# Kernel optimization log

Measured on AMD Instinct MI355X. Metric: run time of the kernel, lower is better.

The kernel has to match this reference:

```python
import jax, jax.numpy as jnp
import numpy as np

BLOCK = 64      # BigBird block size
HEADS = 8
N_GLOBAL = 1
WINDOW = 1      # +/-1 block sliding window
N_RAND = 3


def _build_block_idx(n_blocks, seed=0):
    """Per query block: global + window + random key blocks, causal, deduped, -1 padded."""
    rng = np.random.RandomState(seed)
    m = N_GLOBAL + (2 * WINDOW + 1) + N_RAND  # 7
    idx = np.full((n_blocks, m), -1, np.int32)
    for i in range(n_blocks):
        s = set(range(min(N_GLOBAL, i + 1)))
        for w in range(i - WINDOW, i + 1):  # causal window (blocks <= i)
            if w >= 0:
                s.add(w)
        cand = [c for c in range(i + 1) if c not in s]
        rng.shuffle(cand)
        s.update(cand[:N_RAND])
        ss = sorted(s)
        idx[i, :len(ss)] = ss
    return idx


def setup_inputs() -> dict:
    key = jax.random.key(0)
    ks = jax.random.split(key, 12)
    b, S, D = 4, 4096, 768
    dff = 4 * D
    init = lambda k, shape: (0.02 * jax.random.normal(k, shape, jnp.float32))
    return {
        'q': jax.random.normal(ks[0], (b, S, D), jnp.float32),
        'ln1_g': jnp.ones((D,), jnp.float32), 'ln1_b': jnp.zeros((D,), jnp.float32),
        'Wq': init(ks[1], (D, D)), 'bq': jnp.zeros((D,), jnp.float32),
        'Wk': init(ks[2], (D, D)), 'bk': jnp.zeros((D,), jnp.float32),
        'Wv': init(ks[3], (D, D)), 'bv': jnp.zeros((D,), jnp.float32),
        'Wo': init(ks[4], (D, D)), 'bo': jnp.zeros((D,), jnp.float32),
        'ln2_g': jnp.ones((D,), jnp.float32), 'ln2_b': jnp.zeros((D,), jnp.float32),
        'W1': init(ks[5], (D, dff)), 'b1': jnp.zeros((dff,), jnp.float32),
        'W2': init(ks[6], (dff, D)), 'b2': jnp.zeros((D,), jnp.float32),
        'key_block_idx': jnp.asarray(_build_block_idx(S // BLOCK), jnp.int32),
    }


def _layernorm(x, g, b, eps=1e-5):
    mu = jnp.mean(x, axis=-1, keepdims=True)
    var = jnp.mean(jnp.square(x - mu), axis=-1, keepdims=True)
    return (x - mu) * jax.lax.rsqrt(var + eps) * g + b


def _bigbird_attn(x, Wq, bq, Wk, bk, Wv, bv, Wo, bo, key_block_idx):
    b, S, D = x.shape
    H, hd = HEADS, D // HEADS
    nb = S // BLOCK
    m = key_block_idx.shape[1]
    proj = lambda W, bias: (x @ W + bias).reshape(b, nb, BLOCK, H, hd).transpose(0, 3, 1, 2, 4)
    q = proj(Wq, bq)  # [b,h,nb,B,hd]
    k = proj(Wk, bk)
    v = proj(Wv, bv)
    valid = key_block_idx >= 0                      # [nb, m]
    idx = jnp.maximum(key_block_idx, 0)
    kg = k[:, :, idx]                               # [b,h,nb,m,B,hd]
    vg = v[:, :, idx]
    scores = jnp.einsum('bhnqd,bhnmkd->bhnqmk', q, kg) / jnp.sqrt(jnp.float32(hd))
    off = jnp.arange(BLOCK)
    qpos = jnp.arange(nb)[:, None] * BLOCK + off    # [nb, B]
    kpos = idx[..., None] * BLOCK + off             # [nb, m, B]
    mask = valid[:, :, None] & (kpos[:, None, :, :] <= qpos[:, :, None, None])  # [nb,q,m,k]
    scores = jnp.where(mask[None, None], scores, jnp.float32(-1e9))
    attn = jax.nn.softmax(scores.reshape(b, H, nb, BLOCK, m * BLOCK), axis=-1)
    attn = attn.reshape(b, H, nb, BLOCK, m, BLOCK)
    out = jnp.einsum('bhnqmk,bhnmkd->bhnqd', attn, vg)   # [b,h,nb,B,hd]
    out = out.transpose(0, 2, 3, 1, 4).reshape(b, S, D)
    return out @ Wo + bo


def reference(q, ln1_g, ln1_b, Wq, bq, Wk, bk, Wv, bv, Wo, bo,
              ln2_g, ln2_b, W1, b1, W2, b2, key_block_idx):
    # pre-norm residual: x + attn(ln1(x))
    x = q + _bigbird_attn(_layernorm(q, ln1_g, ln1_b), Wq, bq, Wk, bk, Wv, bv, Wo, bo, key_block_idx)
    h = _layernorm(x, ln2_g, ln2_b)
    x = x + (jax.nn.gelu(h @ W1 + b1) @ W2 + b2)
    return x
```

## Files before the change

kernel.cpp:

```cpp
#include <hip/hip_runtime.h>
#include <cstdint>

typedef __bf16  bf16x8 __attribute__((ext_vector_type(8)));
typedef float   f32x4  __attribute__((ext_vector_type(4)));

__device__ __forceinline__ float bf2f(uint16_t u) {
    uint32_t x = ((uint32_t)u) << 16;
    float f; __builtin_memcpy(&f, &x, 4); return f;
}
__device__ __forceinline__ uint16_t f2bf(float f) {
    uint32_t x; __builtin_memcpy(&x, &f, 4);
    uint32_t r = (x + 0x7fffu + ((x >> 16) & 1u)) >> 16;
    return (uint16_t)r;
}
__device__ __forceinline__ float gelu_f(float x) {
    float y = 0.7978845608028654f * (x + 0.044715f * x * x * x);
    float e = __expf(-2.0f * y);
    return x * __builtin_amdgcn_rcpf(1.0f + e);
}
__device__ __forceinline__ float ldf(const void* p, size_t i, int f) {
    return f ? ((const float*)p)[i] : bf2f(((const uint16_t*)p)[i]);
}

__device__ __forceinline__ void gl_lds16(const void* g, void* lds) {
    __builtin_amdgcn_global_load_lds(
        (const __attribute__((address_space(1))) void*)g,
        (__attribute__((address_space(3))) void*)lds,
        16, 0, 0);
}

#define BATCH 4
#define SEQ   4096
#define DMODEL 768
#define HEADS 8
#define HDIM  96
#define DFF   3072
#define NBLK  64
#define MKEYS 7
#define MROWS 16384

__global__ void sniff_k(const uint32_t* __restrict__ g, int* __restrict__ flag) {
    if (threadIdx.x == 0) flag[0] = (g[0] == 0x3F800000u) ? 1 : 0;
}

__global__ void transpose_k(const void* __restrict__ in, uint16_t* __restrict__ out,
                            int R, int C, const int* __restrict__ flag) {
    __shared__ float t[32][33];
    const int f = flag[0];
    int bx = blockIdx.x * 32, by = blockIdx.y * 32;
    int tx = threadIdx.x, ty = threadIdx.y;
    #pragma unroll
    for (int i = 0; i < 32; i += 8)
        t[ty + i][tx] = ldf(in, (size_t)(by + ty + i) * C + bx + tx, f);
    __syncthreads();
    #pragma unroll
    for (int i = 0; i < 32; i += 8)
        out[(size_t)(bx + ty + i) * R + by + tx] = f2bf(t[tx][ty + i]);
}

__global__ void concat_bias_k(const void* bq, const void* bk, const void* bv,
                              uint16_t* out, const int* __restrict__ flag) {
    const int f = flag[0];
    int i = blockIdx.x * 256 + threadIdx.x;
    if (i < DMODEL) {
        out[i]              = f2bf(ldf(bq, i, f));
        out[DMODEL + i]     = f2bf(ldf(bk, i, f));
        out[2 * DMODEL + i] = f2bf(ldf(bv, i, f));
    }
}

__global__ __launch_bounds__(256) void ln_k(const void* __restrict__ x,
                                            const void* __restrict__ g,
                                            const void* __restrict__ b,
                                            uint16_t* __restrict__ y,
                                            int xmode, const int* __restrict__ flag) {
    const int f = flag[0];
    const int xf = xmode ? f : 0;
    int row = blockIdx.x, tid = threadIdx.x;
    size_t base = (size_t)row * DMODEL;
    float v0 = ldf(x, base + tid, xf);
    float v1 = ldf(x, base + tid + 256, xf);
    float v2 = ldf(x, base + tid + 512, xf);
    float s = v0 + v1 + v2;
    float s2 = v0 * v0 + v1 * v1 + v2 * v2;
    #pragma unroll
    for (int off = 1; off < 64; off <<= 1) {
        s  += __shfl_xor(s, off, 64);
        s2 += __shfl_xor(s2, off, 64);
    }
    __shared__ float rs[4], rs2[4];
    if ((tid & 63) == 0) { rs[tid >> 6] = s; rs2[tid >> 6] = s2; }
    __syncthreads();
    s = rs[0] + rs[1] + rs[2] + rs[3];
    s2 = rs2[0] + rs2[1] + rs2[2] + rs2[3];
    float mu = s * (1.0f / DMODEL);
    float var = s2 * (1.0f / DMODEL) - mu * mu;
    float rstd = rsqrtf(var + 1e-5f);
    uint16_t* yr = y + base;
    yr[tid]       = f2bf((v0 - mu) * rstd * ldf(g, tid, f)       + ldf(b, tid, f));
    yr[tid + 256] = f2bf((v1 - mu) * rstd * ldf(g, tid + 256, f) + ldf(b, tid + 256, f));
    yr[tid + 512] = f2bf((v2 - mu) * rstd * ldf(g, tid + 512, f) + ldf(b, tid + 512, f));
}

template <int EPI>
__global__ __launch_bounds__(512, 4) void gemm128(
        const uint16_t* __restrict__ A, const uint16_t* __restrict__ Bt,
        const void* __restrict__ bias, const void* __restrict__ resid,
        void* __restrict__ C, int M, int N, int K,
        int bmode, int rmode, int omode, const int* __restrict__ flag) {
    __shared__ __align__(16) uint16_t SMEM[36864];
    const int f = flag[0];
    const int bf_ = bmode ? f : 0, rf = rmode ? f : 0, of = omode ? f : 0;
    const int tid = threadIdx.x;
    const int lane = tid & 63, wave = tid >> 6;
    const int l15 = lane & 15, quad = lane >> 4;
    const int wr = wave >> 2, wc = wave & 3;

    const int GX = gridDim.x;
    const int flat = blockIdx.y * GX + blockIdx.x;
    const int xcd = flat & 7, w8 = flat >> 3;
    const int cb = w8 % GX;
    const int rb = (w8 / GX) * 8 + xcd;
    const int m0 = rb * 128, n0 = cb * 256;
    const int NT = K >> 5;

    const uint32_t cxor = ((uint32_t)(quad ^ ((l15 >> 2) & 3))) << 4;
    const uint32_t aA = (uint32_t)((wr * 64 + l15) * 64) + cxor;
    const uint32_t aB = 24576u + (uint32_t)((wc * 64 + l15) * 64) + cxor;
    const char* const smb = (const char*)SMEM;

    const uint32_t goffA = (uint32_t)((tid >> 2) * K + (((tid & 3) ^ ((tid >> 4) & 3)) << 3));

    f32x4 acc[4][4] = {};
    bf16x8 af[4], bfr[4];

    const uint16_t* const Abase = A + (size_t)m0 * K;
    const uint16_t* const Bbase = Bt + (size_t)n0 * K;

    auto stage = [&](int t, int s) {
        const uint16_t* ga = Abase + t * 32 + goffA;
        const uint16_t* gb = Bbase + t * 32 + goffA;
        uint16_t* da = SMEM + s * 4096 + wave * 512;
        uint16_t* db = SMEM + 12288 + s * 8192 + wave * 512;
        gl_lds16(ga, da);
        gl_lds16(gb, db);
        gl_lds16(gb + (size_t)128 * K, db + 4096);
    };

#define LD(S) { _Pragma("unroll") for (int mi = 0; mi < 4; ++mi)                     \
        af[mi] = *(const bf16x8*)(smb + (S) * 8192 + mi * 1024 + aA);                \
      _Pragma("unroll") for (int nj = 0; nj < 4; ++nj)                               \
        bfr[nj] = *(const bf16x8*)(smb + (S) * 16384 + nj * 1024 + aB); }
#define MM { _Pragma("unroll") for (int mi = 0; mi < 4; ++mi)                        \
      _Pragma("unroll") for (int nj = 0; nj < 4; ++nj)                               \
        acc[mi][nj] = __builtin_amdgcn_mfma_f32_16x16x32_bf16(                       \
            af[mi], bfr[nj], acc[mi][nj], 0, 0, 0); }
#define PH(S, T) {                                                                   \
    if ((T) + 2 < NT) stage((T) + 2, ((S) + 2) % 3);                                 \
    LD(S);                                                                           \
    asm volatile("s_waitcnt lgkmcnt(0)" ::: "memory");                               \
    __builtin_amdgcn_sched_barrier(0);                                               \
    __builtin_amdgcn_s_setprio(1);                                                   \
    MM;                                                                              \
    __builtin_amdgcn_s_setprio(0);                                                   \
    __builtin_amdgcn_sched_barrier(0);                                               \
    if ((T) + 2 < NT)      { asm volatile("s_waitcnt vmcnt(3)" ::: "memory"); }      \
    else if ((T) + 1 < NT) { asm volatile("s_waitcnt vmcnt(0)" ::: "memory"); }      \
    asm volatile("s_barrier" ::: "memory"); }

    stage(0, 0);
    stage(1, 1);
    asm volatile("s_waitcnt vmcnt(3)" ::: "memory");
    asm volatile("s_barrier" ::: "memory");

    #pragma unroll 1
    for (int t = 0; t < NT; t += 3) {
        PH(0, t)
        PH(1, t + 1)
        PH(2, t + 2)
    }
#undef LD
#undef MM
#undef PH

    float bv[4];
    #pragma unroll
    for (int nj = 0; nj < 4; ++nj)
        bv[nj] = ldf(bias, n0 + wc * 64 + nj * 16 + l15, bf_);

    #pragma unroll
    for (int mi = 0; mi < 4; ++mi) {
        int rowb = m0 + wr * 64 + mi * 16 + quad * 4;
        #pragma unroll
        for (int nj = 0; nj < 4; ++nj) {
            int col = n0 + wc * 64 + nj * 16 + l15;
            #pragma unroll
            for (int r = 0; r < 4; ++r) {
                float v = acc[mi][nj][r] + bv[nj];
                if (EPI == 2) v = gelu_f(v);
                size_t off = (size_t)(rowb + r) * N + col;
                if (EPI == 1) v += ldf(resid, off, rf);
                if (of) ((float*)C)[off] = v;
                else    ((uint16_t*)C)[off] = f2bf(v);
            }
        }
    }
}

__global__ __launch_bounds__(256, 4) void attn_k(const __bf16* __restrict__ QKV,
                                                 const int* __restrict__ kbi,
                                                 uint16_t* __restrict__ Aout) {
    const int qb = blockIdx.x;
    const int h  = blockIdx.y;
    const int bb = blockIdx.z;
    const int tid = threadIdx.x;
    const int lane = tid & 63, wave = tid >> 6;
    const int l15 = lane & 15, quad = lane >> 4;
    const int h8 = l15 >> 3;

    __shared__ __align__(16) __bf16 Ks[64 * 96];
    __shared__ __align__(16) __bf16 VTs[96 * 72];
    __shared__ __align__(16) __bf16 Ps[4 * 16 * 72];

    char* const ksb = (char*)Ks;
    char* const vtb = (char*)VTs;
    char* const psb = (char*)Ps + wave * 2304;

    const int tq = bb * SEQ + qb * 64;
    const int r0row = wave * 16 + quad * 4;
    const float sc = 0.10206207262f;

    int nv[4];
    #pragma unroll
    for (int r = 0; r < 4; ++r) {
        int cnt = 0;
        #pragma unroll
        for (int m = 0; m < MKEYS; ++m)
            cnt += (kbi[(r0row + r) * MKEYS + m] >= 0) ? 1 : 0;
        nv[r] = cnt;
    }

    bf16x8 aq[3];
    {
        const __bf16* qp = QKV + (size_t)(tq + wave * 16 + l15) * 2304 + h * HDIM + quad * 8;
        aq[0] = *(const bf16x8*)(qp);
        aq[1] = *(const bf16x8*)(qp + 32);
        aq[2] = *(const bf16x8*)(qp + 64);
    }

    uint32_t goff[3], kwb[3], vtw[3];
    #pragma unroll
    for (int i = 0; i < 3; ++i) {
        int c = i * 256 + tid;
        int r = c / 12, cm = c % 12;
        goff[i] = (uint32_t)(r * 2304 + cm * 8);
        kwb[i]  = (uint32_t)(r * 192 + ((cm ^ (r & 3)) << 4));
        vtw[i]  = (uint32_t)(cm * 8 * 144 + ((r * 2) ^ ((cm & 7) << 4)));
    }

    bf16x8 kreg[3], vreg[3];
    auto load_tile = [&](int kb) {
        const __bf16* base = QKV + (size_t)(bb * SEQ + kb * 64) * 2304 + h * HDIM;
        #pragma unroll
        for (int i = 0; i < 3; ++i) {
            kreg[i] = *(const bf16x8*)(base + DMODEL + goff[i]);
            vreg[i] = *(const bf16x8*)(base + 2 * DMODEL + goff[i]);
        }
    };
    auto write_tile = [&]() {
        #pragma unroll
        for (int i = 0; i < 3; ++i) {
            *(bf16x8*)(ksb + kwb[i]) = kreg[i];
            #pragma unroll
            for (int j2 = 0; j2 < 8; ++j2)
                *(__bf16*)(vtb + vtw[i] + j2 * 144) = vreg[i][j2];
        }
    };

    int kb0 = kbi[qb * MKEYS + 0];
    int kb_cur = kb0 < 0 ? 0 : kb0;
    load_tile(kb_cur);
    write_tile();
    __syncthreads();

    float mrun[4] = {-1e30f, -1e30f, -1e30f, -1e30f};
    float lrun[4] = {0.f, 0.f, 0.f, 0.f};
    f32x4 oacc[6] = {};

    const uint32_t kq16 = (uint32_t)((quad ^ (l15 & 3)) << 4);
    const uint32_t prB  = (uint32_t)((quad << 4) ^ ((l15 >> 2) << 4));

    for (int mi = 0; mi < MKEYS; ++mi) {
        int kb_nxt = 0;
        if (mi + 1 < MKEYS) {
            kb_nxt = kbi[qb * MKEYS + mi + 1];
            kb_nxt = kb_nxt < 0 ? 0 : kb_nxt;
            load_tile(kb_nxt);
        }

        f32x4 s[4] = {};
        __builtin_amdgcn_s_setprio(1);
        #pragma unroll
        for (int kt = 0; kt < 3; ++kt) {
            #pragma unroll
            for (int j = 0; j < 4; ++j) {
                bf16x8 bk = *(const bf16x8*)(ksb + (j * 16 + l15) * 192 + kt * 64 + kq16);
                s[j] = __builtin_amdgcn_mfma_f32_16x16x32_bf16(aq[kt], bk, s[j], 0, 0, 0);
            }
        }
        __builtin_amdgcn_s_setprio(0);

        const bool diag = (kb_cur == qb);
        #pragma unroll
        for (int r = 0; r < 4; ++r) {
            const bool rowen = (mi < nv[r]);
            float mx = -1e30f;
            #pragma unroll
            for (int j = 0; j < 4; ++j) {
                float v = s[j][r] * sc;
                if (!rowen || (diag && (j * 16 + l15 > r0row + r))) v = -1e30f;
                s[j][r] = v;
                mx = fmaxf(mx, v);
            }
            #pragma unroll
            for (int off = 1; off < 16; off <<= 1) mx = fmaxf(mx, __shfl_xor(mx, off, 64));
            float mnew = fmaxf(mrun[r], mx);
            float alpha = __expf(mrun[r] - mnew);
            mrun[r] = mnew;
            float ls = 0.f;
            #pragma unroll
            for (int j = 0; j < 4; ++j) {
                float p = __expf(s[j][r] - mnew);
                s[j][r] = p;
                ls += p;
            }
            #pragma unroll
            for (int off = 1; off < 16; off <<= 1) ls += __shfl_xor(ls, off, 64);
            lrun[r] = lrun[r] * alpha + ls;
            #pragma unroll
            for (int t = 0; t < 6; ++t) oacc[t][r] *= alpha;
            #pragma unroll
            for (int j = 0; j < 4; ++j)
                *(__bf16*)(psb + (quad * 4 + r) * 144 +
                           (((uint32_t)(j * 32) | (uint32_t)(l15 * 2)) ^ ((uint32_t)quad << 4)))
                    = (__bf16)s[j][r];
        }

        asm volatile("s_waitcnt lgkmcnt(0)" ::: "memory");
        __builtin_amdgcn_sched_barrier(0);

        __builtin_amdgcn_s_setprio(1);
        #pragma unroll
        for (int kt = 0; kt < 2; ++kt) {
            bf16x8 ap = *(const bf16x8*)(psb + l15 * 144 + kt * 64 + prB);
            #pragma unroll
            for (int t = 0; t < 6; ++t) {
                const uint32_t L = (uint32_t)((((2 * t) & 7) << 4) ^ (kt << 6));
                bf16x8 bv = *(const bf16x8*)(vtb + (t * 16 + l15) * 144 +
                                             ((uint32_t)(quad << 4) ^ (uint32_t)(h8 << 4) ^ L));
                oacc[t] = __builtin_amdgcn_mfma_f32_16x16x32_bf16(ap, bv, oacc[t], 0, 0, 0);
            }
        }
        __builtin_amdgcn_s_setprio(0);

        if (mi + 1 < MKEYS) {
            __syncthreads();
            write_tile();
            __syncthreads();
            kb_cur = kb_nxt;
        }
    }

    #pragma unroll
    for (int r = 0; r < 4; ++r) {
        float inv = 1.0f / lrun[r];
        int token = tq + r0row + r;
        #pragma unroll
        for (int t = 0; t < 6; ++t) {
            int col = h * HDIM + t * 16 + l15;
            Aout[(size_t)token * DMODEL + col] = f2bf(oacc[t][r] * inv);
        }
    }
}

extern "C" void kernel_launch(void* const* d_in, const int* in_sizes, int n_in,
                              void* d_out, int out_size, void* d_ws, size_t ws_size,
                              hipStream_t stream) {
    const void* q     = d_in[0];
    const void* ln1_g = d_in[1];
    const void* ln1_b = d_in[2];
    const void* Wq    = d_in[3];
    const void* bq    = d_in[4];
    const void* Wk    = d_in[5];
    const void* bk    = d_in[6];
    const void* Wv    = d_in[7];
    const void* bv    = d_in[8];
    const void* Wo    = d_in[9];
    const void* bo    = d_in[10];
    const void* ln2_g = d_in[11];
    const void* ln2_b = d_in[12];
    const void* W1    = d_in[13];
    const void* b1    = d_in[14];
    const void* W2    = d_in[15];
    const void* b2    = d_in[16];
    const int*  kbi   = (const int*)d_in[17];
    char* ws = (char*)d_ws;

    uint16_t* WqkvT = (uint16_t*)(ws + 0);
    uint16_t* WoT   = (uint16_t*)(ws + 3538944);
    uint16_t* W1T   = (uint16_t*)(ws + 4718592);
    uint16_t* W2T   = (uint16_t*)(ws + 9437184);
    uint16_t* bqkv  = (uint16_t*)(ws + 14155776);
    int*      flag  = (int*)(ws + 14160384);
    uint16_t* x1    = (uint16_t*)(ws + 14160896);
    uint16_t* QKV   = (uint16_t*)(ws + 39326720);
    uint16_t* attn  = (uint16_t*)(ws + 114824192);
    uint16_t* xb    = (uint16_t*)(ws + 139990016);
    uint16_t* mid   = QKV;

    sniff_k<<<1, 64, 0, stream>>>((const uint32_t*)ln1_g, flag);

    dim3 tb(32, 8);
    transpose_k<<<dim3(24, 24), tb, 0, stream>>>(Wq, WqkvT, DMODEL, DMODEL, flag);
    transpose_k<<<dim3(24, 24), tb, 0, stream>>>(Wk, WqkvT + DMODEL * DMODEL, DMODEL, DMODEL, flag);
    transpose_k<<<dim3(24, 24), tb, 0, stream>>>(Wv, WqkvT + 2 * DMODEL * DMODEL, DMODEL, DMODEL, flag);
    transpose_k<<<dim3(24, 24), tb, 0, stream>>>(Wo, WoT, DMODEL, DMODEL, flag);
    transpose_k<<<dim3(96, 24), tb, 0, stream>>>(W1, W1T, DMODEL, DFF, flag);
    transpose_k<<<dim3(24, 96), tb, 0, stream>>>(W2, W2T, DFF, DMODEL, flag);
    concat_bias_k<<<3, 256, 0, stream>>>(bq, bk, bv, bqkv, flag);

    ln_k<<<MROWS, 256, 0, stream>>>(q, ln1_g, ln1_b, x1, 1, flag);
    gemm128<0><<<dim3(9, 128), 512, 0, stream>>>(x1, WqkvT, bqkv, nullptr, QKV,
                                                 MROWS, 3 * DMODEL, DMODEL, 0, 0, 0, flag);
    attn_k<<<dim3(NBLK, HEADS, BATCH), 256, 0, stream>>>((const __bf16*)QKV, kbi, attn);
    gemm128<1><<<dim3(3, 128), 512, 0, stream>>>(attn, WoT, bo, q, xb,
                                                 MROWS, DMODEL, DMODEL, 1, 1, 0, flag);
    ln_k<<<MROWS, 256, 0, stream>>>(xb, ln2_g, ln2_b, x1, 0, flag);
    gemm128<2><<<dim3(12, 128), 512, 0, stream>>>(x1, W1T, b1, nullptr, mid,
                                                  MROWS, DFF, DMODEL, 1, 0, 0, flag);
    gemm128<1><<<dim3(3, 128), 512, 0, stream>>>(mid, W2T, b2, xb, d_out,
                                                 MROWS, DMODEL, DFF, 1, 0, 1, flag);
}
```

Measured before the change: 586.3 us.

## Restructure GEMM to 128x128 tiles with 64-deep K steps and split A/B staging

Replaces the 512-thread 128x256 GEMM with a 256-thread 128x128 tile kernel that loads 64-wide K slices per stage. A is triple-buffered and B double-buffered, with a new XOR swizzle and two MFMA passes per stage. This halves the barriers per K element and doubles the block count per GEMM, aiming for better latency hiding and occupancy. The trade-off is less B reuse per tile and more LDS per block.

```diff
diff --git a/kernel.cpp b/kernel.cpp
--- a/kernel.cpp
+++ b/kernel.cpp
@@ -103,83 +103,105 @@
 }
 
 template <int EPI>
-__global__ __launch_bounds__(512, 4) void gemm128(
+__global__ __launch_bounds__(256, 2) void gemmP(
         const uint16_t* __restrict__ A, const uint16_t* __restrict__ Bt,
         const void* __restrict__ bias, const void* __restrict__ resid,
         void* __restrict__ C, int M, int N, int K,
         int bmode, int rmode, int omode, const int* __restrict__ flag) {
-    __shared__ __align__(16) uint16_t SMEM[36864];
+    __shared__ __align__(16) uint16_t SMEM[40960];
     const int f = flag[0];
     const int bf_ = bmode ? f : 0, rf = rmode ? f : 0, of = omode ? f : 0;
     const int tid = threadIdx.x;
     const int lane = tid & 63, wave = tid >> 6;
     const int l15 = lane & 15, quad = lane >> 4;
-    const int wr = wave >> 2, wc = wave & 3;
+    const int wr = wave >> 1, wc = wave & 1;
 
     const int GX = gridDim.x;
     const int flat = blockIdx.y * GX + blockIdx.x;
     const int xcd = flat & 7, w8 = flat >> 3;
     const int cb = w8 % GX;
     const int rb = (w8 / GX) * 8 + xcd;
-    const int m0 = rb * 128, n0 = cb * 256;
-    const int NT = K >> 5;
-
-    const uint32_t cxor = ((uint32_t)(quad ^ ((l15 >> 2) & 3))) << 4;
-    const uint32_t aA = (uint32_t)((wr * 64 + l15) * 64) + cxor;
-    const uint32_t aB = 24576u + (uint32_t)((wc * 64 + l15) * 64) + cxor;
+    const int m0 = rb * 128, n0 = cb * 128;
+    const int NT = K >> 6;
+
+    const uint32_t v = ((uint32_t)l15 >> 1) & 7u;
+    const uint32_t tka = (((uint32_t)quad ^ v) << 4);
+    const uint32_t tkb = ((((uint32_t)quad + 4u) ^ v) << 4);
+    const uint32_t aA0 = (uint32_t)((wr * 64 + l15) * 128) + tka;
+    const uint32_t aA1 = (uint32_t)((wr * 64 + l15) * 128) + tkb;
+    const uint32_t aB0 = 49152u + (uint32_t)((wc * 64 + l15) * 128) + tka;
+    const uint32_t aB1 = 49152u + (uint32_t)((wc * 64 + l15) * 128) + tkb;
     const char* const smb = (const char*)SMEM;
-
-    const uint32_t goffA = (uint32_t)((tid >> 2) * K + (((tid & 3) ^ ((tid >> 4) & 3)) << 3));
-
-    f32x4 acc[4][4] = {};
-    bf16x8 af[4], bfr[4];
+    char* const smw = (char*)SMEM;
+
+    const uint32_t goff = (uint32_t)((tid >> 3) * K + (((tid & 7) ^ ((tid >> 4) & 7)) << 3));
 
     const uint16_t* const Abase = A + (size_t)m0 * K;
     const uint16_t* const Bbase = Bt + (size_t)n0 * K;
 
-    auto stage = [&](int t, int s) {
-        const uint16_t* ga = Abase + t * 32 + goffA;
-        const uint16_t* gb = Bbase + t * 32 + goffA;
-        uint16_t* da = SMEM + s * 4096 + wave * 512;
-        uint16_t* db = SMEM + 12288 + s * 8192 + wave * 512;
-        gl_lds16(ga, da);
-        gl_lds16(gb, db);
-        gl_lds16(gb + (size_t)128 * K, db + 4096);
+    f32x4 acc[4][4] = {};
+    bf16x8 af0[4], bf0[4], af1[4], bf1[4];
+
+    auto stageA = [&](int kt, int s) {
+        const uint16_t* g = Abase + (size_t)kt * 64 + goff;
+        char* d = smw + s * 16384 + wave * 1024;
+        #pragma unroll
+        for (int it = 0; it < 4; ++it)
+            gl_lds16(g + (size_t)(it * 32) * K, d + it * 4096);
     };
-
-#define LD(S) { _Pragma("unroll") for (int mi = 0; mi < 4; ++mi)                     \
-        af[mi] = *(const bf16x8*)(smb + (S) * 8192 + mi * 1024 + aA);                \
-      _Pragma("unroll") for (int nj = 0; nj < 4; ++nj)                               \
-        bfr[nj] = *(const bf16x8*)(smb + (S) * 16384 + nj * 1024 + aB); }
-#define MM { _Pragma("unroll") for (int mi = 0; mi < 4; ++mi)                        \
-      _Pragma("unroll") for (int nj = 0; nj < 4; ++nj)                               \
-        acc[mi][nj] = __builtin_amdgcn_mfma_f32_16x16x32_bf16(                       \
-            af[mi], bfr[nj], acc[mi][nj], 0, 0, 0); }
-#define PH(S, T) {                                                                   \
-    if ((T) + 2 < NT) stage((T) + 2, ((S) + 2) % 3);                                 \
-    LD(S);                                                                           \
-    asm volatile("s_waitcnt lgkmcnt(0)" ::: "memory");                               \
-    __builtin_amdgcn_sched_barrier(0);                                               \
-    __builtin_amdgcn_s_setprio(1);                                                   \
-    MM;                                                                              \
-    __builtin_amdgcn_s_setprio(0);                                                   \
-    __builtin_amdgcn_sched_barrier(0);                                               \
-    if ((T) + 2 < NT)      { asm volatile("s_waitcnt vmcnt(3)" ::: "memory"); }      \
-    else if ((T) + 1 < NT) { asm volatile("s_waitcnt vmcnt(0)" ::: "memory"); }      \
-    asm volatile("s_barrier" ::: "memory"); }
-
-    stage(0, 0);
-    stage(1, 1);
-    asm volatile("s_waitcnt vmcnt(3)" ::: "memory");
+    auto stageB = [&](int kt, int s) {
+        const uint16_t* g = Bbase + (size_t)kt * 64 + goff;
+        char* d = smw + 49152 + s * 16384 + wave * 1024;
+        #pragma unroll
+        for (int it = 0; it < 4; ++it)
+            gl_lds16(g + (size_t)(it * 32) * K, d + it * 4096);
+    };
+
+#define RD(SA, SB) {                                                                \
+    _Pragma("unroll") for (int mi = 0; mi < 4; ++mi)                                \
+        af0[mi] = *(const bf16x8*)(smb + (SA) * 16384 + mi * 2048 + aA0);           \
+    _Pragma("unroll") for (int nj = 0; nj < 4; ++nj)                                \
+        bf0[nj] = *(const bf16x8*)(smb + (SB) * 16384 + nj * 2048 + aB0);           \
+    _Pragma("unroll") for (int mi = 0; mi < 4; ++mi)                                \
+        af1[mi] = *(const bf16x8*)(smb + (SA) * 16384 + mi * 2048 + aA1);           \
+    _Pragma("unroll") for (int nj = 0; nj < 4; ++nj)                                \
+        bf1[nj] = *(const bf16x8*)(smb + (SB) * 16384 + nj * 2048 + aB1); }
+#define MM {                                                                        \
+    _Pragma("unroll") for (int mi = 0; mi < 4; ++mi)                                \
+    _Pragma("unroll") for (int nj = 0; nj < 4; ++nj)                                \
+        acc[mi][nj] = __builtin_amdgcn_mfma_f32_16x16x32_bf16(                      \
+            af0[mi], bf0[nj], acc[mi][nj], 0, 0, 0);                                \
+    _Pragma("unroll") for (int mi = 0; mi < 4; ++mi)                                \
+    _Pragma("unroll") for (int nj = 0; nj < 4; ++nj)                                \
+        acc[mi][nj] = __builtin_amdgcn_mfma_f32_16x16x32_bf16(                      \
+            af1[mi], bf1[nj], acc[mi][nj], 0, 0, 0); }
+#define PH(KK) {                                                                    \
+    const int T = t + (KK);                                                         \
+    RD((KK) % 3, (KK) & 1);                                                         \
+    __builtin_amdgcn_sched_barrier(0);                                              \
+    if (T + 1 < NT) stageB(T + 1, ((KK) + 1) & 1);                                  \
+    if (T + 2 < NT) stageA(T + 2, ((KK) + 2) % 3);                                  \
+    asm volatile("s_waitcnt lgkmcnt(0)" ::: "memory");                              \
+    __builtin_amdgcn_sched_barrier(0);                                              \
+    __builtin_amdgcn_s_setprio(1);                                                  \
+    MM;                                                                             \
+    __builtin_amdgcn_s_setprio(0);                                                  \
+    __builtin_amdgcn_sched_barrier(0);                                              \
+    if (T + 2 < NT)      { asm volatile("s_waitcnt vmcnt(4)" ::: "memory"); }       \
+    else if (T + 1 < NT) { asm volatile("s_waitcnt vmcnt(0)" ::: "memory"); }       \
+    if (T + 1 < NT)      { asm volatile("s_barrier" ::: "memory"); } }
+
+    stageA(0, 0);
+    stageB(0, 0);
+    stageA(1, 1);
+    asm volatile("s_waitcnt vmcnt(4)" ::: "memory");
     asm volatile("s_barrier" ::: "memory");
 
     #pragma unroll 1
-    for (int t = 0; t < NT; t += 3) {
-        PH(0, t)
-        PH(1, t + 1)
-        PH(2, t + 2)
-    }
-#undef LD
+    for (int t = 0; t < NT; t += 6) {
+        PH(0) PH(1) PH(2) PH(3) PH(4) PH(5)
+    }
+#undef RD
 #undef MM
 #undef PH
 
@@ -196,12 +218,12 @@
             int col = n0 + wc * 64 + nj * 16 + l15;
             #pragma unroll
             for (int r = 0; r < 4; ++r) {
-                float v = acc[mi][nj][r] + bv[nj];
-                if (EPI == 2) v = gelu_f(v);
+                float val = acc[mi][nj][r] + bv[nj];
+                if (EPI == 2) val = gelu_f(val);
                 size_t off = (size_t)(rowb + r) * N + col;
-                if (EPI == 1) v += ldf(resid, off, rf);
-                if (of) ((float*)C)[off] = v;
-                else    ((uint16_t*)C)[off] = f2bf(v);
+                if (EPI == 1) val += ldf(resid, off, rf);
+                if (of) ((float*)C)[off] = val;
+                else    ((uint16_t*)C)[off] = f2bf(val);
             }
         }
     }
@@ -317,10 +339,10 @@
             float mx = -1e30f;
             #pragma unroll
             for (int j = 0; j < 4; ++j) {
-                float v = s[j][r] * sc;
-                if (!rowen || (diag && (j * 16 + l15 > r0row + r))) v = -1e30f;
-                s[j][r] = v;
-                mx = fmaxf(mx, v);
+                float vv = s[j][r] * sc;
+                if (!rowen || (diag && (j * 16 + l15 > r0row + r))) vv = -1e30f;
+                s[j][r] = vv;
+                mx = fmaxf(mx, vv);
             }
             #pragma unroll
             for (int off = 1; off < 16; off <<= 1) mx = fmaxf(mx, __shfl_xor(mx, off, 64));
@@ -430,14 +452,14 @@
     concat_bias_k<<<3, 256, 0, stream>>>(bq, bk, bv, bqkv, flag);
 
     ln_k<<<MROWS, 256, 0, stream>>>(q, ln1_g, ln1_b, x1, 1, flag);
-    gemm128<0><<<dim3(9, 128), 512, 0, stream>>>(x1, WqkvT, bqkv, nullptr, QKV,
-                                                 MROWS, 3 * DMODEL, DMODEL, 0, 0, 0, flag);
+    gemmP<0><<<dim3(18, 128), 256, 0, stream>>>(x1, WqkvT, bqkv, nullptr, QKV,
+                                                MROWS, 3 * DMODEL, DMODEL, 0, 0, 0, flag);
     attn_k<<<dim3(NBLK, HEADS, BATCH), 256, 0, stream>>>((const __bf16*)QKV, kbi, attn);
-    gemm128<1><<<dim3(3, 128), 512, 0, stream>>>(attn, WoT, bo, q, xb,
-                                                 MROWS, DMODEL, DMODEL, 1, 1, 0, flag);
+    gemmP<1><<<dim3(6, 128), 256, 0, stream>>>(attn, WoT, bo, q, xb,
+                                               MROWS, DMODEL, DMODEL, 1, 1, 0, flag);
     ln_k<<<MROWS, 256, 0, stream>>>(xb, ln2_g, ln2_b, x1, 0, flag);
-    gemm128<2><<<dim3(12, 128), 512, 0, stream>>>(x1, W1T, b1, nullptr, mid,
-                                                  MROWS, DFF, DMODEL, 1, 0, 0, flag);
-    gemm128<1><<<dim3(3, 128), 512, 0, stream>>>(mid, W2T, b2, xb, d_out,
-                                                 MROWS, DMODEL, DFF, 1, 0, 1, flag);
-}
+    gemmP<2><<<dim3(24, 128), 256, 0, stream>>>(x1, W1T, b1, nullptr, mid,
+                                                MROWS, DFF, DMODEL, 1, 0, 0, flag);
+    gemmP<1><<<dim3(6, 128), 256, 0, stream>>>(mid, W2T, b2, xb, d_out,
+                                               MROWS, DMODEL, DFF, 1, 0, 1, flag);
+}
```

Result: slower. 654.6 us (+11.6%).
